# Optimization experiments

Hardware: AMD Instinct MI355X
Metric: run time of the kernel (lower is better)

Reference implementation:

```python
import jax, jax.numpy as jnp
import numpy as np

B, F, K, D = 512, 2048, 64, 16


def setup_inputs() -> dict:
    key = jax.random.key(0)
    k1, k2 = jax.random.split(key)
    x = jax.random.normal(k1, (B, F), dtype=jnp.float32)
    # glorot-uniform-ish init for the projection kernel [F, K, D]
    limit = np.sqrt(6.0 / (F + K * D)).astype(np.float32)
    kernel = jax.random.uniform(k2, (F, K, D), dtype=jnp.float32, minval=-limit, maxval=limit)
    return {"x": x, "kernel": kernel}


def reference(x, kernel):
    # activation: [B, K, D]
    act = jnp.einsum('bf,fkd->bkd', x, kernel)
    # pairwise L1 distance over D: diffs [B, K, D, B] -> abs_diffs [B, K, B]
    diffs = act[:, :, :, None] - jnp.transpose(act, (1, 2, 0))[None, :, :, :]
    abs_diffs = jnp.sum(jnp.abs(diffs), axis=2)
    # exp-similarity summed over the other batch elements (includes self: +1)
    feats = jnp.sum(jnp.exp(-abs_diffs), axis=2)  # [B, K]
    return jnp.concatenate([x, feats], axis=1)  # [B, F + K]
```

## Files before the change

### kernel.cpp

```cpp
#include <hip/hip_runtime.h>

#define B_   512
#define F_   2048
#define K_   64
#define D_   16
#define N_   1024
#define OUTW (F_+K_)
#define LOG2E 1.44269504088896340736f

typedef __attribute__((ext_vector_type(8))) short short8;
typedef __attribute__((ext_vector_type(4))) float f32x4;

__device__ __forceinline__ ushort f2bf(float f) {
    union { float f; unsigned u; } un; un.f = f;
    unsigned u = un.u;
    u += 0x7FFF + ((u >> 16) & 1);
    return (ushort)(u >> 16);
}

__device__ __forceinline__ float exp2_neg(float x) {
    float r;
    asm("v_exp_f32 %0, -%1" : "=v"(r) : "v"(x));
    return r;
}

__global__ __launch_bounds__(256) void prep_kernel(const float* __restrict__ x,
                                                   const float* __restrict__ w,
                                                   float* __restrict__ out,
                                                   ushort* __restrict__ xb,
                                                   ushort* __restrict__ wt) {
    __shared__ float t[32][33];
    const int blk = blockIdx.x;
    const int tid = threadIdx.x;
    if (blk < 1024) {
        const int i = blk * 256 + tid;
        float4 v = ((const float4*)x)[i];
        const int b = i >> 9, c = i & 511;
        ((float4*)out)[b * (OUTW / 4) + c] = v;
        ushort4 u = make_ushort4(f2bf(v.x * LOG2E), f2bf(v.y * LOG2E),
                                 f2bf(v.z * LOG2E), f2bf(v.w * LOG2E));
        ((ushort4*)xb)[i] = u;
    } else {
        const int r  = tid >> 3;
        const int c4 = (tid & 7) * 4;
        #pragma unroll 1
        for (int i = 0; i < 8; ++i) {
            const int tb = (blk - 1024) * 8 + i;
            const int f0 = (tb >> 5) * 32, n0 = (tb & 31) * 32;
            float4 v = *(const float4*)(w + (size_t)(f0 + r) * N_ + n0 + c4);
            __syncthreads();
            t[r][c4 + 0] = v.x; t[r][c4 + 1] = v.y;
            t[r][c4 + 2] = v.z; t[r][c4 + 3] = v.w;
            __syncthreads();
            ushort4 u = make_ushort4(f2bf(t[c4 + 0][r]), f2bf(t[c4 + 1][r]),
                                     f2bf(t[c4 + 2][r]), f2bf(t[c4 + 3][r]));
            *(ushort4*)(wt + (size_t)(n0 + r) * F_ + f0 + c4) = u;
        }
    }
}

__global__ __launch_bounds__(256) void gemm_mfma_kernel(const ushort* __restrict__ xb,
                                                        const ushort* __restrict__ wt,
                                                        float* __restrict__ actp) {
    const int bm0 = blockIdx.x * 64;
    const int bn0 = blockIdx.y * 32;
    const int f0  = blockIdx.z * 512;
    const int tid = threadIdx.x;
    const int l   = tid & 63;
    const int w   = tid >> 6;
    const int mw  = (w >> 1) * 32;
    const int nw  = (w & 1) * 16;
    const int lr  = l & 15;
    const int lk  = (l >> 4) * 8;

    const ushort* pa0 = xb + (size_t)(bm0 + mw + lr) * F_ + f0 + lk;
    const ushort* pa1 = pa0 + 16 * F_;
    const ushort* pb0 = wt + (size_t)(bn0 + nw + lr) * F_ + f0 + lk;

    f32x4 acc0 = {}, acc1 = {};
    #pragma unroll 4
    for (int kk = 0; kk < 512; kk += 32) {
        short8 a0 = *(const short8*)(pa0 + kk);
        short8 a1 = *(const short8*)(pa1 + kk);
        short8 b0 = *(const short8*)(pb0 + kk);
        acc0 = __builtin_amdgcn_mfma_f32_16x16x32_bf16(a0, b0, acc0, 0, 0, 0);
        acc1 = __builtin_amdgcn_mfma_f32_16x16x32_bf16(a1, b0, acc1, 0, 0, 0);
    }

    const int n = bn0 + nw + lr;
    const int k = n >> 4, d = n & 15;
    const int mbase = bm0 + mw + (l >> 4) * 4;
    float* dst = actp + (size_t)blockIdx.z * (K_ * B_ * D_) + (size_t)k * (B_ * D_) + d;
    #pragma unroll
    for (int r = 0; r < 4; ++r) {
        dst[(size_t)(mbase + r) * D_]      = acc0[r];
        dst[(size_t)(mbase + 16 + r) * D_] = acc1[r];
    }
}

__global__ __launch_bounds__(512) void pairwise_kernel(const float* __restrict__ actp,
                                                       float* __restrict__ out) {
    __shared__ float s_act[B_ * D_];
    __shared__ float red[8][64];

    const int bt = blockIdx.x;
    const int k  = blockIdx.y;
    const int tid  = threadIdx.x;
    const int lane = tid & 63;
    const int wave = tid >> 6;

    const f32x4* p0 = (const f32x4*)(actp + (size_t)k * (B_ * D_));
    const f32x4* p1 = p0 + (K_ * B_ * D_) / 4;
    const f32x4* p2 = p1 + (K_ * B_ * D_) / 4;
    const f32x4* p3 = p2 + (K_ * B_ * D_) / 4;
    #pragma unroll
    for (int i = 0; i < 4; ++i) {
        const int idx = tid + i * 512;
        ((f32x4*)s_act)[idx] = (p0[idx] + p1[idx]) + (p2[idx] + p3[idx]);
    }
    __syncthreads();

    const int b = bt * 64 + lane;
    const float4* arow = (const float4*)&s_act[b * D_];
    const float4 a0 = arow[0], a1 = arow[1], a2 = arow[2], a3 = arow[3];

    float p0a = 0.0f, p1a = 0.0f;
    const int b2lo = wave * 64;
    #pragma unroll 2
    for (int b2 = b2lo; b2 < b2lo + 64; b2 += 2) {
        {
            const float4* v = (const float4*)&s_act[b2 * D_];
            const float4 v0 = v[0], v1 = v[1], v2 = v[2], v3 = v[3];
            float t0 = fabsf(a0.x - v0.x) + fabsf(a0.y - v0.y);
            float t1 = fabsf(a0.z - v0.z) + fabsf(a0.w - v0.w);
            float t2 = fabsf(a1.x - v1.x) + fabsf(a1.y - v1.y);
            float t3 = fabsf(a1.z - v1.z) + fabsf(a1.w - v1.w);
            float t4 = fabsf(a2.x - v2.x) + fabsf(a2.y - v2.y);
            float t5 = fabsf(a2.z - v2.z) + fabsf(a2.w - v2.w);
            float t6 = fabsf(a3.x - v3.x) + fabsf(a3.y - v3.y);
            float t7 = fabsf(a3.z - v3.z) + fabsf(a3.w - v3.w);
            float s = ((t0 + t1) + (t2 + t3)) + ((t4 + t5) + (t6 + t7));
            p0a += exp2_neg(s);
        }
        {
            const float4* v = (const float4*)&s_act[(b2 + 1) * D_];
            const float4 v0 = v[0], v1 = v[1], v2 = v[2], v3 = v[3];
            float t0 = fabsf(a0.x - v0.x) + fabsf(a0.y - v0.y);
            float t1 = fabsf(a0.z - v0.z) + fabsf(a0.w - v0.w);
            float t2 = fabsf(a1.x - v1.x) + fabsf(a1.y - v1.y);
            float t3 = fabsf(a1.z - v1.z) + fabsf(a1.w - v1.w);
            float t4 = fabsf(a2.x - v2.x) + fabsf(a2.y - v2.y);
            float t5 = fabsf(a2.z - v2.z) + fabsf(a2.w - v2.w);
            float t6 = fabsf(a3.x - v3.x) + fabsf(a3.y - v3.y);
            float t7 = fabsf(a3.z - v3.z) + fabsf(a3.w - v3.w);
            float s = ((t0 + t1) + (t2 + t3)) + ((t4 + t5) + (t6 + t7));
            p1a += exp2_neg(s);
        }
    }

    red[wave][lane] = p0a + p1a;
    __syncthreads();
    if (wave == 0) {
        float total = 0.0f;
        #pragma unroll
        for (int i = 0; i < 8; ++i) total += red[i][lane];
        out[(size_t)b * OUTW + F_ + k] = total;
    }
}

extern "C" void kernel_launch(void* const* d_in, const int* in_sizes, int n_in,
                              void* d_out, int out_size, void* d_ws, size_t ws_size,
                              hipStream_t stream) {
    const float* x = (const float*)d_in[0];
    const float* wsrc = (const float*)d_in[1];
    float* out = (float*)d_out;

    ushort* xb   = (ushort*)d_ws;
    ushort* wt   = (ushort*)((char*)d_ws + (size_t)2 * 1024 * 1024);
    float*  actp = (float*)((char*)d_ws + (size_t)6 * 1024 * 1024);

    prep_kernel<<<1280, 256, 0, stream>>>(x, wsrc, out, xb, wt);
    gemm_mfma_kernel<<<dim3(8, 32, 4), 256, 0, stream>>>(xb, wt, actp);
    pairwise_kernel<<<dim3(8, K_), 512, 0, stream>>>(actp, out);
}
```

Measured before the change: 120.6 us.

## Tile GEMM through swizzled LDS double buffer, atomic split-K, fp16 pairwise math

The GEMM now stages 64x64 bf16 tiles of A and B in double-buffered, XOR-swizzled shared memory and computes a 2x2 grid of MFMA tiles per wave, so each global load is reused across more MFMAs. Split-K partial sums are combined with atomicAdd into a single zeroed activation buffer instead of four partial buffers, which removes the 4-way summation in the pairwise kernel but adds a memset and atomic traffic. The pairwise L1 distance now uses packed half2 subtract, abs and add to double arithmetic throughput, at the cost of fp16 precision in the distances.

```diff
diff --git a/kernel.cpp b/kernel.cpp
--- a/kernel.cpp
+++ b/kernel.cpp
@@ -1,4 +1,5 @@
 #include <hip/hip_runtime.h>
+#include <hip/hip_fp16.h>
 
 #define B_   512
 #define F_   2048
@@ -7,6 +8,10 @@
 #define N_   1024
 #define OUTW (F_+K_)
 #define LOG2E 1.44269504088896340736f
+#define KSPLIT 4
+#define KCH  (F_/KSPLIT)
+#define BK   64
+#define NSTEP (KCH/BK)
 
 typedef __attribute__((ext_vector_type(8))) short short8;
 typedef __attribute__((ext_vector_type(4))) float f32x4;
@@ -61,46 +66,90 @@
 
 __global__ __launch_bounds__(256) void gemm_mfma_kernel(const ushort* __restrict__ xb,
                                                         const ushort* __restrict__ wt,
-                                                        float* __restrict__ actp) {
+                                                        float* __restrict__ act) {
+    __shared__ ushort As[2][64 * 64];
+    __shared__ ushort Bs[2][64 * 64];
+
     const int bm0 = blockIdx.x * 64;
-    const int bn0 = blockIdx.y * 32;
-    const int f0  = blockIdx.z * 512;
+    const int bn0 = blockIdx.y * 64;
+    const int f0  = blockIdx.z * KCH;
     const int tid = threadIdx.x;
     const int l   = tid & 63;
     const int w   = tid >> 6;
     const int mw  = (w >> 1) * 32;
-    const int nw  = (w & 1) * 16;
+    const int nw  = (w & 1) * 32;
     const int lr  = l & 15;
-    const int lk  = (l >> 4) * 8;
-
-    const ushort* pa0 = xb + (size_t)(bm0 + mw + lr) * F_ + f0 + lk;
-    const ushort* pa1 = pa0 + 16 * F_;
-    const ushort* pb0 = wt + (size_t)(bn0 + nw + lr) * F_ + f0 + lk;
-
-    f32x4 acc0 = {}, acc1 = {};
-    #pragma unroll 4
-    for (int kk = 0; kk < 512; kk += 32) {
-        short8 a0 = *(const short8*)(pa0 + kk);
-        short8 a1 = *(const short8*)(pa1 + kk);
-        short8 b0 = *(const short8*)(pb0 + kk);
-        acc0 = __builtin_amdgcn_mfma_f32_16x16x32_bf16(a0, b0, acc0, 0, 0, 0);
-        acc1 = __builtin_amdgcn_mfma_f32_16x16x32_bf16(a1, b0, acc1, 0, 0, 0);
-    }
-
-    const int n = bn0 + nw + lr;
-    const int k = n >> 4, d = n & 15;
-    const int mbase = bm0 + mw + (l >> 4) * 4;
-    float* dst = actp + (size_t)blockIdx.z * (K_ * B_ * D_) + (size_t)k * (B_ * D_) + d;
+    const int lkc = l >> 4;
+    const int sw  = lr & 7;
+
+    const int r0 = tid >> 2;
+    const int c0 = (tid & 3) * 2;
+    const int c1 = c0 + 1;
+    const ushort* gA0 = xb + (size_t)(bm0 + r0) * F_ + f0 + c0 * 8;
+    const ushort* gA1 = gA0 + 8;
+    const ushort* gB0 = wt + (size_t)(bn0 + r0) * F_ + f0 + c0 * 8;
+    const ushort* gB1 = gB0 + 8;
+    const int wA0 = r0 * 64 + ((c0 ^ (r0 & 7)) * 8);
+    const int wA1 = r0 * 64 + ((c1 ^ (r0 & 7)) * 8);
+
+    f32x4 acc00 = {}, acc01 = {}, acc10 = {}, acc11 = {};
+
+    uint4 a0v = *(const uint4*)gA0;
+    uint4 a1v = *(const uint4*)gA1;
+    uint4 b0v = *(const uint4*)gB0;
+    uint4 b1v = *(const uint4*)gB1;
+    *(uint4*)&As[0][wA0] = a0v; *(uint4*)&As[0][wA1] = a1v;
+    *(uint4*)&Bs[0][wA0] = b0v; *(uint4*)&Bs[0][wA1] = b1v;
+    __syncthreads();
+
     #pragma unroll
-    for (int r = 0; r < 4; ++r) {
-        dst[(size_t)(mbase + r) * D_]      = acc0[r];
-        dst[(size_t)(mbase + 16 + r) * D_] = acc1[r];
-    }
-}
-
-__global__ __launch_bounds__(512) void pairwise_kernel(const float* __restrict__ actp,
+    for (int s = 0; s < NSTEP; ++s) {
+        const int cur = s & 1, nxt = cur ^ 1;
+        if (s < NSTEP - 1) {
+            a0v = *(const uint4*)(gA0 + (s + 1) * BK);
+            a1v = *(const uint4*)(gA1 + (s + 1) * BK);
+            b0v = *(const uint4*)(gB0 + (s + 1) * BK);
+            b1v = *(const uint4*)(gB1 + (s + 1) * BK);
+        }
+        #pragma unroll
+        for (int ks = 0; ks < 2; ++ks) {
+            const int cb = ks * 4 + lkc;
+            short8 a_0 = *(const short8*)&As[cur][(mw + lr) * 64      + ((cb ^ sw) * 8)];
+            short8 a_1 = *(const short8*)&As[cur][(mw + 16 + lr) * 64 + ((cb ^ sw) * 8)];
+            short8 b_0 = *(const short8*)&Bs[cur][(nw + lr) * 64      + ((cb ^ sw) * 8)];
+            short8 b_1 = *(const short8*)&Bs[cur][(nw + 16 + lr) * 64 + ((cb ^ sw) * 8)];
+            acc00 = __builtin_amdgcn_mfma_f32_16x16x32_bf16(a_0, b_0, acc00, 0, 0, 0);
+            acc01 = __builtin_amdgcn_mfma_f32_16x16x32_bf16(a_0, b_1, acc01, 0, 0, 0);
+            acc10 = __builtin_amdgcn_mfma_f32_16x16x32_bf16(a_1, b_0, acc10, 0, 0, 0);
+            acc11 = __builtin_amdgcn_mfma_f32_16x16x32_bf16(a_1, b_1, acc11, 0, 0, 0);
+        }
+        if (s < NSTEP - 1) {
+            *(uint4*)&As[nxt][wA0] = a0v; *(uint4*)&As[nxt][wA1] = a1v;
+            *(uint4*)&Bs[nxt][wA0] = b0v; *(uint4*)&Bs[nxt][wA1] = b1v;
+        }
+        __syncthreads();
+    }
+
+    #pragma unroll
+    for (int mi = 0; mi < 2; ++mi) {
+        #pragma unroll
+        for (int ni = 0; ni < 2; ++ni) {
+            const f32x4 a = (mi == 0) ? (ni == 0 ? acc00 : acc01)
+                                      : (ni == 0 ? acc10 : acc11);
+            const int n = bn0 + nw + ni * 16 + lr;
+            const int k = n >> 4, d = n & 15;
+            const int mbase = bm0 + mw + mi * 16 + lkc * 4;
+            float* dst = act + ((size_t)k * B_ + mbase) * D_ + d;
+            #pragma unroll
+            for (int r = 0; r < 4; ++r)
+                atomicAdd(dst + r * D_, a[r]);
+        }
+    }
+}
+
+__global__ __launch_bounds__(512) void pairwise_kernel(const float* __restrict__ act,
                                                        float* __restrict__ out) {
-    __shared__ float s_act[B_ * D_];
+    __shared__ __half2 s2[B_ * D_ / 2];
     __shared__ float red[8][64];
 
     const int bt = blockIdx.x;
@@ -109,56 +158,46 @@
     const int lane = tid & 63;
     const int wave = tid >> 6;
 
-    const f32x4* p0 = (const f32x4*)(actp + (size_t)k * (B_ * D_));
-    const f32x4* p1 = p0 + (K_ * B_ * D_) / 4;
-    const f32x4* p2 = p1 + (K_ * B_ * D_) / 4;
-    const f32x4* p3 = p2 + (K_ * B_ * D_) / 4;
+    const f32x4* src = (const f32x4*)(act + (size_t)k * (B_ * D_));
     #pragma unroll
     for (int i = 0; i < 4; ++i) {
         const int idx = tid + i * 512;
-        ((f32x4*)s_act)[idx] = (p0[idx] + p1[idx]) + (p2[idx] + p3[idx]);
+        f32x4 v = src[idx];
+        s2[idx * 2]     = __floats2half2_rn(v[0], v[1]);
+        s2[idx * 2 + 1] = __floats2half2_rn(v[2], v[3]);
+    }
+    const int b = bt * 64 + lane;
+    __half2 ar[8];
+    {
+        const f32x4* arow = (const f32x4*)(act + ((size_t)k * B_ + b) * D_);
+        #pragma unroll
+        for (int i = 0; i < 4; ++i) {
+            f32x4 v = arow[i];
+            ar[i * 2]     = __floats2half2_rn(v[0], v[1]);
+            ar[i * 2 + 1] = __floats2half2_rn(v[2], v[3]);
+        }
     }
     __syncthreads();
 
-    const int b = bt * 64 + lane;
-    const float4* arow = (const float4*)&s_act[b * D_];
-    const float4 a0 = arow[0], a1 = arow[1], a2 = arow[2], a3 = arow[3];
-
-    float p0a = 0.0f, p1a = 0.0f;
+    float p = 0.0f;
     const int b2lo = wave * 64;
-    #pragma unroll 2
-    for (int b2 = b2lo; b2 < b2lo + 64; b2 += 2) {
-        {
-            const float4* v = (const float4*)&s_act[b2 * D_];
-            const float4 v0 = v[0], v1 = v[1], v2 = v[2], v3 = v[3];
-            float t0 = fabsf(a0.x - v0.x) + fabsf(a0.y - v0.y);
-            float t1 = fabsf(a0.z - v0.z) + fabsf(a0.w - v0.w);
-            float t2 = fabsf(a1.x - v1.x) + fabsf(a1.y - v1.y);
-            float t3 = fabsf(a1.z - v1.z) + fabsf(a1.w - v1.w);
-            float t4 = fabsf(a2.x - v2.x) + fabsf(a2.y - v2.y);
-            float t5 = fabsf(a2.z - v2.z) + fabsf(a2.w - v2.w);
-            float t6 = fabsf(a3.x - v3.x) + fabsf(a3.y - v3.y);
-            float t7 = fabsf(a3.z - v3.z) + fabsf(a3.w - v3.w);
-            float s = ((t0 + t1) + (t2 + t3)) + ((t4 + t5) + (t6 + t7));
-            p0a += exp2_neg(s);
-        }
-        {
-            const float4* v = (const float4*)&s_act[(b2 + 1) * D_];
-            const float4 v0 = v[0], v1 = v[1], v2 = v[2], v3 = v[3];
-            float t0 = fabsf(a0.x - v0.x) + fabsf(a0.y - v0.y);
-            float t1 = fabsf(a0.z - v0.z) + fabsf(a0.w - v0.w);
-            float t2 = fabsf(a1.x - v1.x) + fabsf(a1.y - v1.y);
-            float t3 = fabsf(a1.z - v1.z) + fabsf(a1.w - v1.w);
-            float t4 = fabsf(a2.x - v2.x) + fabsf(a2.y - v2.y);
-            float t5 = fabsf(a2.z - v2.z) + fabsf(a2.w - v2.w);
-            float t6 = fabsf(a3.x - v3.x) + fabsf(a3.y - v3.y);
-            float t7 = fabsf(a3.z - v3.z) + fabsf(a3.w - v3.w);
-            float s = ((t0 + t1) + (t2 + t3)) + ((t4 + t5) + (t6 + t7));
-            p1a += exp2_neg(s);
-        }
-    }
-
-    red[wave][lane] = p0a + p1a;
+    #pragma unroll 4
+    for (int b2 = b2lo; b2 < b2lo + 64; ++b2) {
+        const __half2* vr = &s2[b2 * 8];
+        __half2 sA = __habs2(__hsub2(ar[0], vr[0]));
+        __half2 sB = __habs2(__hsub2(ar[1], vr[1]));
+        sA = __hadd2(sA, __habs2(__hsub2(ar[2], vr[2])));
+        sB = __hadd2(sB, __habs2(__hsub2(ar[3], vr[3])));
+        sA = __hadd2(sA, __habs2(__hsub2(ar[4], vr[4])));
+        sB = __hadd2(sB, __habs2(__hsub2(ar[5], vr[5])));
+        sA = __hadd2(sA, __habs2(__hsub2(ar[6], vr[6])));
+        sB = __hadd2(sB, __habs2(__hsub2(ar[7], vr[7])));
+        sA = __hadd2(sA, sB);
+        const float dist = __low2float(sA) + __high2float(sA);
+        p += exp2_neg(dist);
+    }
+
+    red[wave][lane] = p;
     __syncthreads();
     if (wave == 0) {
         float total = 0.0f;
@@ -175,11 +214,12 @@
     const float* wsrc = (const float*)d_in[1];
     float* out = (float*)d_out;
 
-    ushort* xb   = (ushort*)d_ws;
-    ushort* wt   = (ushort*)((char*)d_ws + (size_t)2 * 1024 * 1024);
-    float*  actp = (float*)((char*)d_ws + (size_t)6 * 1024 * 1024);
-
+    ushort* xb  = (ushort*)d_ws;
+    ushort* wt  = (ushort*)((char*)d_ws + (size_t)2 * 1024 * 1024);
+    float*  act = (float*)((char*)d_ws + (size_t)6 * 1024 * 1024);
+
+    hipMemsetAsync(act, 0, (size_t)K_ * B_ * D_ * sizeof(float), stream);
     prep_kernel<<<1280, 256, 0, stream>>>(x, wsrc, out, xb, wt);
-    gemm_mfma_kernel<<<dim3(8, 32, 4), 256, 0, stream>>>(xb, wt, actp);
-    pairwise_kernel<<<dim3(8, K_), 512, 0, stream>>>(actp, out);
-}
+    gemm_mfma_kernel<<<dim3(8, 16, KSPLIT), 256, 0, stream>>>(xb, wt, act);
+    pairwise_kernel<<<dim3(8, K_), 512, 0, stream>>>(act, out);
+}
```

Measured after the change: 103.2 us. 14.5% less time.
